# Optimization experiments

Measured on AMD Instinct MI355X. Metric: run time of the kernel, lower is better.

## Reference

```python
import jax, jax.numpy as jnp
import numpy as np

EPS = 1e-12  # tf.math.l2_normalize epsilon

def _l2norm(x):
    # normalize over last axis, matching K.l2_normalize semantics
    sq = jnp.sum(x * x, axis=-1, keepdims=True)
    return x * jax.lax.rsqrt(jnp.maximum(sq, EPS))

def setup_inputs() -> dict:
    key = jax.random.key(0)
    k1, k2, k3 = jax.random.split(key, 3)
    B, L, D, P = 16, 256, 256, 20
    sent1 = jax.random.normal(k1, (B, L, D), dtype=jnp.float32)
    sent2 = jax.random.normal(k2, (B, L, D), dtype=jnp.float32)
    # glorot_uniform for shape (P, D)
    limit = np.sqrt(6.0 / (P + D)).astype(np.float32)
    kernel = jax.random.uniform(k3, (P, D), minval=-limit, maxval=limit, dtype=jnp.float32)
    return {"sent1": sent1, "sent2": sent2, "kernel": kernel}

def reference(sent1, sent2, kernel):
    # sent1: [B,L1,D], sent2: [B,L2,D], kernel: [P,D]
    v1 = _l2norm(sent1[:, :, None, :] * kernel)  # [B,L1,P,D]
    v2 = _l2norm(sent2[:, :, None, :] * kernel)  # [B,L2,P,D]
    # per-perspective cosine similarity matrix: [B,L1,L2,P]
    cos = jnp.einsum('blpd,bmpd->blmp', v1, v2)
    # max over the other sentence's positions (L2) -> [B,L1,P]
    return jnp.max(cos, axis=2)
```

## Files before the change

### kernel.cpp

```cpp
#include <hip/hip_runtime.h>
#include <hip/hip_bf16.h>


#define B_DIM 16
#define L_DIM 256
#define D_DIM 256
#define P_DIM 20
#define EPS 1e-12f
#define LDP 264

typedef __attribute__((ext_vector_type(8))) __bf16 bf16x8;
typedef __attribute__((ext_vector_type(4))) float f32x4;

__device__ __forceinline__ unsigned short f2bf(float x) {
  unsigned int u = __float_as_uint(x);
  u += 0x7fffu + ((u >> 16) & 1u);
  return (unsigned short)(u >> 16);
}

__global__ __launch_bounds__(256)
void prep2(const float* __restrict__ s1, const float* __restrict__ s2,
           const float* __restrict__ kg,
           float* __restrict__ rn1, float* __restrict__ rn2,
           unsigned short* __restrict__ s1bf, unsigned short* __restrict__ s2bf) {
  __shared__ __align__(16) unsigned short QA[32 * LDP];
  __shared__ __align__(16) unsigned short QB[32 * LDP];
  const int tid = threadIdx.x, lane = tid & 63, wave = tid >> 6;
  const int lr = lane & 15, q = lane >> 4;
  const int sent = blockIdx.x & 1, t = blockIdx.x >> 1;
  const int r0 = t * 32, b = r0 >> 8;
  const float* src = sent ? s2 : s1;
  unsigned short* sbf = sent ? s2bf : s1bf;
  float* rn = sent ? rn2 : rn1;

  #pragma unroll
  for (int i = 0; i < 8; ++i) {
    const int row = i * 4 + wave;
    float4 sv = *(const float4*)(src + (size_t)(r0 + row) * D_DIM + lane * 4);
    unsigned int c0 = ((unsigned int)f2bf(sv.y) << 16) | f2bf(sv.x);
    unsigned int c1 = ((unsigned int)f2bf(sv.w) << 16) | f2bf(sv.z);
    *(uint2*)&sbf[(size_t)(r0 + row) * D_DIM + lane * 4] = make_uint2(c0, c1);
    unsigned int q0 = ((unsigned int)f2bf(sv.y * sv.y) << 16) | f2bf(sv.x * sv.x);
    unsigned int q1 = ((unsigned int)f2bf(sv.w * sv.w) << 16) | f2bf(sv.z * sv.z);
    *(uint2*)&QA[row * LDP + lane * 4] = make_uint2(q0, q1);
  }
  #pragma unroll
  for (int j = 0; j < 5; ++j) {
    const int row = wave * 5 + j;
    float4 kv = *(const float4*)(kg + row * D_DIM + lane * 4);
    unsigned int c0 = ((unsigned int)f2bf(kv.y * kv.y) << 16) | f2bf(kv.x * kv.x);
    unsigned int c1 = ((unsigned int)f2bf(kv.w * kv.w) << 16) | f2bf(kv.z * kv.z);
    *(uint2*)&QB[row * LDP + lane * 4] = make_uint2(c0, c1);
  }
  __syncthreads();

  const int mt = wave & 1, nt = wave >> 1;
  f32x4 acc = {0.f, 0.f, 0.f, 0.f};
  #pragma unroll
  for (int ks = 0; ks < 8; ++ks) {
    const int cc = ks * 4 + q;
    bf16x8 a  = *(const bf16x8*)&QA[(mt * 16 + lr) * LDP + cc * 8];
    bf16x8 bb = *(const bf16x8*)&QB[(nt * 16 + lr) * LDP + cc * 8];
    acc = __builtin_amdgcn_mfma_f32_16x16x32_bf16(a, bb, acc, 0, 0, 0);
  }
  const int p = nt * 16 + lr;
  if (p < P_DIM) {
    #pragma unroll
    for (int r = 0; r < 4; ++r) {
      const int l = (r0 & 255) + mt * 16 + q * 4 + r;
      rn[((size_t)b * P_DIM + p) * L_DIM + l] = rsqrtf(fmaxf(acc[r], EPS));
    }
  }
}

__global__ __launch_bounds__(256, 2)
void mpm_main(const unsigned short* __restrict__ s1bf,
              const unsigned short* __restrict__ s2bf,
              const float* __restrict__ kg, const float* __restrict__ rn1,
              const float* __restrict__ rn2, float* __restrict__ outg) {
  __shared__ __align__(16) unsigned short X1[32 * 256];
  __shared__ float Wout[4 * 32];

  const int tid = threadIdx.x, lane = tid & 63, wave = tid >> 6;
  const int lr = lane & 15, q = lane >> 4;
  const int bid = blockIdx.x;
  const int pgi = bid & 3, lt = (bid >> 2) & 7, b = bid >> 5;
  const int l0 = lt * 32;

  bf16x8 areg[4][8];
  {
    const unsigned short* s2b = s2bf + (size_t)b * L_DIM * D_DIM;
    #pragma unroll
    for (int mi = 0; mi < 4; ++mi) {
      const unsigned short* rp = s2b + (size_t)(wave * 64 + mi * 16 + lr) * D_DIM + q * 8;
      #pragma unroll
      for (int ks = 0; ks < 8; ++ks)
        areg[mi][ks] = *(const bf16x8*)(rp + ks * 32);
    }
  }

  uint2 s1r[8];
  {
    const unsigned short* s1b = s1bf + ((size_t)b * L_DIM + l0) * D_DIM;
    #pragma unroll
    for (int i = 0; i < 8; ++i)
      s1r[i] = *(const uint2*)(s1b + (size_t)(i * 4 + wave) * D_DIM + lane * 4);
  }

  #pragma unroll 1
  for (int pp = 0; pp < 5; ++pp) {
    const int p = pgi * 5 + pp;

    {
      float4 kv = *(const float4*)(kg + p * D_DIM + lane * 4);
      const float k0 = kv.x * kv.x, k1 = kv.y * kv.y, k2 = kv.z * kv.z, k3 = kv.w * kv.w;
      const float* rn1b = rn1 + ((size_t)b * P_DIM + p) * L_DIM + l0;
      #pragma unroll
      for (int i = 0; i < 8; ++i) {
        const int row = i * 4 + wave;
        const float rv = rn1b[row];
        float x0 = __uint_as_float(s1r[i].x << 16)         * k0 * rv;
        float x1 = __uint_as_float(s1r[i].x & 0xffff0000u) * k1 * rv;
        float x2 = __uint_as_float(s1r[i].y << 16)         * k2 * rv;
        float x3 = __uint_as_float(s1r[i].y & 0xffff0000u) * k3 * rv;
        unsigned int c0 = ((unsigned int)f2bf(x1) << 16) | f2bf(x0);
        unsigned int c1 = ((unsigned int)f2bf(x3) << 16) | f2bf(x2);
        *(uint2*)&X1[row * 256 + (((lane >> 1) ^ row) << 3) + ((lane & 1) << 2)] =
            make_uint2(c0, c1);
      }
    }
    __syncthreads();

    f32x4 acc[4][2];
    #pragma unroll
    for (int mi = 0; mi < 4; ++mi) {
      acc[mi][0] = (f32x4){0.f, 0.f, 0.f, 0.f};
      acc[mi][1] = (f32x4){0.f, 0.f, 0.f, 0.f};
    }
    #pragma unroll
    for (int ks = 0; ks < 8; ++ks) {
      const int cc = ks * 4 + q;
      bf16x8 b0 = *(const bf16x8*)&X1[(lr)      * 256 + ((cc ^ lr) << 3)];
      bf16x8 b1 = *(const bf16x8*)&X1[(16 + lr) * 256 + ((cc ^ (16 + lr)) << 3)];
      #pragma unroll
      for (int mi = 0; mi < 4; ++mi) {
        acc[mi][0] = __builtin_amdgcn_mfma_f32_16x16x32_bf16(areg[mi][ks], b0, acc[mi][0], 0, 0, 0);
        acc[mi][1] = __builtin_amdgcn_mfma_f32_16x16x32_bf16(areg[mi][ks], b1, acc[mi][1], 0, 0, 0);
      }
    }

    float4 r2[4];
    {
      const float* rn2b = rn2 + ((size_t)b * P_DIM + p) * L_DIM + wave * 64;
      #pragma unroll
      for (int mi = 0; mi < 4; ++mi)
        r2[mi] = *(const float4*)(rn2b + mi * 16 + q * 4);
    }
    float v[2];
    #pragma unroll
    for (int li = 0; li < 2; ++li) {
      float t = -3.4e38f;
      #pragma unroll
      for (int mi = 0; mi < 4; ++mi) {
        t = fmaxf(t, acc[mi][li][0] * r2[mi].x);
        t = fmaxf(t, acc[mi][li][1] * r2[mi].y);
        t = fmaxf(t, acc[mi][li][2] * r2[mi].z);
        t = fmaxf(t, acc[mi][li][3] * r2[mi].w);
      }
      t = fmaxf(t, __shfl_xor(t, 16));
      t = fmaxf(t, __shfl_xor(t, 32));
      v[li] = t;
    }
    if (q == 0) {
      Wout[wave * 32 + lr]      = v[0];
      Wout[wave * 32 + 16 + lr] = v[1];
    }
    __syncthreads();
    if (tid < 32) {
      float o = fmaxf(fmaxf(Wout[tid], Wout[32 + tid]),
                      fmaxf(Wout[64 + tid], Wout[96 + tid]));
      outg[((size_t)b * L_DIM + (l0 + tid)) * P_DIM + p] = o;
    }
  }
}

extern "C" void kernel_launch(void* const* d_in, const int* in_sizes, int n_in,
                              void* d_out, int out_size, void* d_ws, size_t ws_size,
                              hipStream_t stream) {
  const float* s1 = (const float*)d_in[0];
  const float* s2 = (const float*)d_in[1];
  const float* kg = (const float*)d_in[2];
  float* out = (float*)d_out;

  float* rn1 = (float*)d_ws;
  float* rn2 = rn1 + (size_t)B_DIM * P_DIM * L_DIM;
  unsigned short* s2bf = (unsigned short*)(rn2 + (size_t)B_DIM * P_DIM * L_DIM);
  unsigned short* s1bf = s2bf + (size_t)B_DIM * L_DIM * D_DIM;

  prep2<<<dim3(256), dim3(256), 0, stream>>>(s1, s2, kg, rn1, rn2, s1bf, s2bf);
  mpm_main<<<dim3(512), dim3(256), 0, stream>>>(s1bf, s2bf, kg, rn1, rn2, out);
}
```

Measured before the change: 85.45 us.

## Fuse norm-prep kernel into main kernel, recomputing norms per block

Removes the separate prep kernel that converted inputs to bf16 and computed per-perspective inverse norms into workspace. The main kernel now reads fp32 inputs directly, converts them to bf16 in registers, and computes the inverse norms for its five perspectives with extra MFMAs into shared memory. This drops a kernel launch and the workspace round-trip. In exchange, s2 is read as fp32 (twice the bytes) by every block, and the s2 norm computation is repeated across the 8 blocks sharing a batch and perspective group.

```diff
diff --git a/kernel.cpp b/kernel.cpp
--- a/kernel.cpp
+++ b/kernel.cpp
@@ -7,10 +7,11 @@
 #define D_DIM 256
 #define P_DIM 20
 #define EPS 1e-12f
-#define LDP 264
 
 typedef __attribute__((ext_vector_type(8))) __bf16 bf16x8;
 typedef __attribute__((ext_vector_type(4))) float f32x4;
+
+union frag_cast { uint4 u; bf16x8 v; };
 
 __device__ __forceinline__ unsigned short f2bf(float x) {
   unsigned int u = __float_as_uint(x);
@@ -18,68 +19,28 @@
   return (unsigned short)(u >> 16);
 }
 
-__global__ __launch_bounds__(256)
-void prep2(const float* __restrict__ s1, const float* __restrict__ s2,
-           const float* __restrict__ kg,
-           float* __restrict__ rn1, float* __restrict__ rn2,
-           unsigned short* __restrict__ s1bf, unsigned short* __restrict__ s2bf) {
-  __shared__ __align__(16) unsigned short QA[32 * LDP];
-  __shared__ __align__(16) unsigned short QB[32 * LDP];
-  const int tid = threadIdx.x, lane = tid & 63, wave = tid >> 6;
-  const int lr = lane & 15, q = lane >> 4;
-  const int sent = blockIdx.x & 1, t = blockIdx.x >> 1;
-  const int r0 = t * 32, b = r0 >> 8;
-  const float* src = sent ? s2 : s1;
-  unsigned short* sbf = sent ? s2bf : s1bf;
-  float* rn = sent ? rn2 : rn1;
-
-  #pragma unroll
-  for (int i = 0; i < 8; ++i) {
-    const int row = i * 4 + wave;
-    float4 sv = *(const float4*)(src + (size_t)(r0 + row) * D_DIM + lane * 4);
-    unsigned int c0 = ((unsigned int)f2bf(sv.y) << 16) | f2bf(sv.x);
-    unsigned int c1 = ((unsigned int)f2bf(sv.w) << 16) | f2bf(sv.z);
-    *(uint2*)&sbf[(size_t)(r0 + row) * D_DIM + lane * 4] = make_uint2(c0, c1);
-    unsigned int q0 = ((unsigned int)f2bf(sv.y * sv.y) << 16) | f2bf(sv.x * sv.x);
-    unsigned int q1 = ((unsigned int)f2bf(sv.w * sv.w) << 16) | f2bf(sv.z * sv.z);
-    *(uint2*)&QA[row * LDP + lane * 4] = make_uint2(q0, q1);
-  }
-  #pragma unroll
-  for (int j = 0; j < 5; ++j) {
-    const int row = wave * 5 + j;
-    float4 kv = *(const float4*)(kg + row * D_DIM + lane * 4);
-    unsigned int c0 = ((unsigned int)f2bf(kv.y * kv.y) << 16) | f2bf(kv.x * kv.x);
-    unsigned int c1 = ((unsigned int)f2bf(kv.w * kv.w) << 16) | f2bf(kv.z * kv.z);
-    *(uint2*)&QB[row * LDP + lane * 4] = make_uint2(c0, c1);
-  }
-  __syncthreads();
-
-  const int mt = wave & 1, nt = wave >> 1;
-  f32x4 acc = {0.f, 0.f, 0.f, 0.f};
-  #pragma unroll
-  for (int ks = 0; ks < 8; ++ks) {
-    const int cc = ks * 4 + q;
-    bf16x8 a  = *(const bf16x8*)&QA[(mt * 16 + lr) * LDP + cc * 8];
-    bf16x8 bb = *(const bf16x8*)&QB[(nt * 16 + lr) * LDP + cc * 8];
-    acc = __builtin_amdgcn_mfma_f32_16x16x32_bf16(a, bb, acc, 0, 0, 0);
-  }
-  const int p = nt * 16 + lr;
-  if (p < P_DIM) {
-    #pragma unroll
-    for (int r = 0; r < 4; ++r) {
-      const int l = (r0 & 255) + mt * 16 + q * 4 + r;
-      rn[((size_t)b * P_DIM + p) * L_DIM + l] = rsqrtf(fmaxf(acc[r], EPS));
-    }
-  }
+__device__ __forceinline__ unsigned int sq2(unsigned int w) {
+  float lo = __uint_as_float(w << 16);
+  float hi = __uint_as_float(w & 0xffff0000u);
+  return (unsigned int)f2bf(lo * lo) | ((unsigned int)f2bf(hi * hi) << 16);
+}
+
+__device__ __forceinline__ bf16x8 square_frag(bf16x8 a) {
+  frag_cast in, out;
+  in.v = a;
+  out.u.x = sq2(in.u.x); out.u.y = sq2(in.u.y);
+  out.u.z = sq2(in.u.z); out.u.w = sq2(in.u.w);
+  return out.v;
 }
 
 __global__ __launch_bounds__(256, 2)
-void mpm_main(const unsigned short* __restrict__ s1bf,
-              const unsigned short* __restrict__ s2bf,
-              const float* __restrict__ kg, const float* __restrict__ rn1,
-              const float* __restrict__ rn2, float* __restrict__ outg) {
+void mpm_fused(const float* __restrict__ s1, const float* __restrict__ s2,
+               const float* __restrict__ kg, float* __restrict__ outg) {
   __shared__ __align__(16) unsigned short X1[32 * 256];
-  __shared__ float Wout[4 * 32];
+  __shared__ __align__(16) unsigned short KQ[5 * 264];
+  __shared__ __align__(16) float RN2[5][260];
+  __shared__ float RN1[5][32];
+  __shared__ float Wout[128];
 
   const int tid = threadIdx.x, lane = tid & 63, wave = tid >> 6;
   const int lr = lane & 15, q = lane >> 4;
@@ -89,36 +50,93 @@
 
   bf16x8 areg[4][8];
   {
-    const unsigned short* s2b = s2bf + (size_t)b * L_DIM * D_DIM;
+    const float* s2b = s2 + (size_t)b * L_DIM * D_DIM;
     #pragma unroll
     for (int mi = 0; mi < 4; ++mi) {
-      const unsigned short* rp = s2b + (size_t)(wave * 64 + mi * 16 + lr) * D_DIM + q * 8;
-      #pragma unroll
-      for (int ks = 0; ks < 8; ++ks)
-        areg[mi][ks] = *(const bf16x8*)(rp + ks * 32);
+      const float* rp = s2b + (size_t)(wave * 64 + mi * 16 + lr) * D_DIM + q * 8;
+      #pragma unroll
+      for (int ks = 0; ks < 8; ++ks) {
+        float4 u = *(const float4*)(rp + ks * 32);
+        float4 w = *(const float4*)(rp + ks * 32 + 4);
+        frag_cast f;
+        f.u.x = (unsigned int)f2bf(u.x) | ((unsigned int)f2bf(u.y) << 16);
+        f.u.y = (unsigned int)f2bf(u.z) | ((unsigned int)f2bf(u.w) << 16);
+        f.u.z = (unsigned int)f2bf(w.x) | ((unsigned int)f2bf(w.y) << 16);
+        f.u.w = (unsigned int)f2bf(w.z) | ((unsigned int)f2bf(w.w) << 16);
+        areg[mi][ks] = f.v;
+      }
     }
   }
 
   uint2 s1r[8];
   {
-    const unsigned short* s1b = s1bf + ((size_t)b * L_DIM + l0) * D_DIM;
-    #pragma unroll
-    for (int i = 0; i < 8; ++i)
-      s1r[i] = *(const uint2*)(s1b + (size_t)(i * 4 + wave) * D_DIM + lane * 4);
-  }
+    const float* s1b = s1 + ((size_t)b * L_DIM + l0) * D_DIM;
+    #pragma unroll
+    for (int i = 0; i < 8; ++i) {
+      const int row = i * 4 + wave;
+      float4 sv = *(const float4*)(s1b + (size_t)row * D_DIM + lane * 4);
+      uint2 pk;
+      pk.x = (unsigned int)f2bf(sv.x) | ((unsigned int)f2bf(sv.y) << 16);
+      pk.y = (unsigned int)f2bf(sv.z) | ((unsigned int)f2bf(sv.w) << 16);
+      s1r[i] = pk;
+      uint2 sq = make_uint2(sq2(pk.x), sq2(pk.y));
+      *(uint2*)&X1[row * 256 + (((lane >> 1) ^ row) << 3) + ((lane & 1) << 2)] = sq;
+    }
+  }
+
+  for (int r = wave; r < 5; r += 4) {
+    float4 kv = *(const float4*)(kg + (size_t)(pgi * 5 + r) * D_DIM + lane * 4);
+    uint2 pk;
+    pk.x = (unsigned int)f2bf(kv.x * kv.x) | ((unsigned int)f2bf(kv.y * kv.y) << 16);
+    pk.y = (unsigned int)f2bf(kv.z * kv.z) | ((unsigned int)f2bf(kv.w * kv.w) << 16);
+    *(uint2*)&KQ[r * 264 + lane * 4] = pk;
+  }
+  __syncthreads();
+
+  #pragma unroll
+  for (int mi = 0; mi < 4; ++mi) {
+    f32x4 nacc = {0.f, 0.f, 0.f, 0.f};
+    #pragma unroll
+    for (int ks = 0; ks < 8; ++ks) {
+      bf16x8 asq = square_frag(areg[mi][ks]);
+      bf16x8 bq = *(const bf16x8*)&KQ[lr * 264 + (ks * 4 + q) * 8];
+      nacc = __builtin_amdgcn_mfma_f32_16x16x32_bf16(asq, bq, nacc, 0, 0, 0);
+    }
+    if (lr < 5) {
+      #pragma unroll
+      for (int r = 0; r < 4; ++r)
+        RN2[lr][wave * 64 + mi * 16 + q * 4 + r] = rsqrtf(fmaxf(nacc[r], EPS));
+    }
+  }
+  if (wave < 2) {
+    const int ti = wave, row = ti * 16 + lr;
+    f32x4 nacc = {0.f, 0.f, 0.f, 0.f};
+    #pragma unroll
+    for (int ks = 0; ks < 8; ++ks) {
+      const int cc = ks * 4 + q;
+      bf16x8 asq = *(const bf16x8*)&X1[row * 256 + ((cc ^ row) << 3)];
+      bf16x8 bq  = *(const bf16x8*)&KQ[lr * 264 + cc * 8];
+      nacc = __builtin_amdgcn_mfma_f32_16x16x32_bf16(asq, bq, nacc, 0, 0, 0);
+    }
+    if (lr < 5) {
+      #pragma unroll
+      for (int r = 0; r < 4; ++r)
+        RN1[lr][ti * 16 + q * 4 + r] = rsqrtf(fmaxf(nacc[r], EPS));
+    }
+  }
+  __syncthreads();
 
   #pragma unroll 1
   for (int pp = 0; pp < 5; ++pp) {
     const int p = pgi * 5 + pp;
 
     {
-      float4 kv = *(const float4*)(kg + p * D_DIM + lane * 4);
+      float4 kv = *(const float4*)(kg + (size_t)p * D_DIM + lane * 4);
       const float k0 = kv.x * kv.x, k1 = kv.y * kv.y, k2 = kv.z * kv.z, k3 = kv.w * kv.w;
-      const float* rn1b = rn1 + ((size_t)b * P_DIM + p) * L_DIM + l0;
       #pragma unroll
       for (int i = 0; i < 8; ++i) {
         const int row = i * 4 + wave;
-        const float rv = rn1b[row];
+        const float rv = RN1[pp][row];
         float x0 = __uint_as_float(s1r[i].x << 16)         * k0 * rv;
         float x1 = __uint_as_float(s1r[i].x & 0xffff0000u) * k1 * rv;
         float x2 = __uint_as_float(s1r[i].y << 16)         * k2 * rv;
@@ -150,12 +168,9 @@
     }
 
     float4 r2[4];
-    {
-      const float* rn2b = rn2 + ((size_t)b * P_DIM + p) * L_DIM + wave * 64;
-      #pragma unroll
-      for (int mi = 0; mi < 4; ++mi)
-        r2[mi] = *(const float4*)(rn2b + mi * 16 + q * 4);
-    }
+    #pragma unroll
+    for (int mi = 0; mi < 4; ++mi)
+      r2[mi] = *(const float4*)&RN2[pp][wave * 64 + mi * 16 + q * 4];
     float v[2];
     #pragma unroll
     for (int li = 0; li < 2; ++li) {
@@ -191,12 +206,5 @@
   const float* s2 = (const float*)d_in[1];
   const float* kg = (const float*)d_in[2];
   float* out = (float*)d_out;
-
-  float* rn1 = (float*)d_ws;
-  float* rn2 = rn1 + (size_t)B_DIM * P_DIM * L_DIM;
-  unsigned short* s2bf = (unsigned short*)(rn2 + (size_t)B_DIM * P_DIM * L_DIM);
-  unsigned short* s1bf = s2bf + (size_t)B_DIM * L_DIM * D_DIM;
-
-  prep2<<<dim3(256), dim3(256), 0, stream>>>(s1, s2, kg, rn1, rn2, s1bf, s2bf);
-  mpm_main<<<dim3(512), dim3(256), 0, stream>>>(s1bf, s2bf, kg, rn1, rn2, out);
-}
+  mpm_fused<<<dim3(512), dim3(256), 0, stream>>>(s1, s2, kg, out);
+}
```

Measured after the change: 124.8 us. +46.0%, slower.
